# Kernel optimization log

Hardware: AMD Instinct MI355X
Metric: run time of the kernel (lower is better)

## Reference

```python
import jax, jax.numpy as jnp
import numpy as np

N, E, B, A = 50000, 1600000, 16, 4096
DIN, D, K = 32, 64, 50
EPS_BN = 1e-5


def setup_inputs() -> dict:
    key = jax.random.key(0)
    ks = iter(jax.random.split(key, 80))
    def rn(shape, s=0.05):
        return jax.random.normal(next(ks), shape, jnp.float32) * s
    inp = {
        "x": jax.random.normal(next(ks), (N, DIN), jnp.float32),
        "edge_index": jax.random.randint(next(ks), (2, E), 0, N),
        "action_edges": jax.random.randint(next(ks), (B, A, 2), 0, N),
        "army_counts": jax.random.normal(next(ks), (B, A), jnp.float32),
        "edge_mask": jnp.ones((B, A), jnp.bool_),
    }
    def bn(prefix, c):
        inp[prefix + "_g"] = 1.0 + rn((c,))
        inp[prefix + "_b"] = rn((c,))
        inp[prefix + "_m"] = rn((c,))
        inp[prefix + "_v"] = 1.0 + jax.random.uniform(next(ks), (c,), jnp.float32) * 0.1
    for i, cin in ((1, DIN), (2, D), (3, D)):
        inp[f"s{i}_wl"] = rn((cin, D), 0.1)
        inp[f"s{i}_bl"] = rn((D,))
        inp[f"s{i}_wr"] = rn((cin, D), 0.1)
        bn(f"s{i}_bn", D)
    inp["pl_w1"] = rn((D, 32), 0.1); inp["pl_b1"] = rn((32,)); bn("pl_bn", 32)
    inp["pl_w2"] = rn((32, 1), 0.1); inp["pl_b2"] = rn((1,))
    inp["es_w1"] = rn((2 * D, 64), 0.1); inp["es_b1"] = rn((64,)); bn("es_bn", 64)
    inp["es_w2"] = rn((64, 1), 0.1); inp["es_b2"] = rn((1,))
    inp["as_w1"] = rn((2 * D, 64), 0.1); inp["as_b1"] = rn((64,)); bn("as_bn", 64)
    inp["as_w2"] = rn((64, K), 0.1); inp["as_b2"] = rn((K,))
    return inp


def _bn(h, g, b, m, v):
    # BatchNorm1d in eval mode (running stats); dropout is identity in eval
    return (h - m) * jax.lax.rsqrt(v + EPS_BN) * g + b


def _sage_layer(h, src, dst, wl, bl, wr, g, b, m, v):
    # PyG SAGEConv(mean aggr, normalize=True): out = lin_l(mean_j x_j) + lin_r(x)
    msum = jax.ops.segment_sum(h[src], dst, num_segments=N)          # [N, din]
    cnt = jax.ops.segment_sum(jnp.ones((src.shape[0], 1), h.dtype), dst, num_segments=N)
    mean = msum / jnp.maximum(cnt, 1.0)
    out = mean @ wl + bl + h @ wr                                     # [N, D]
    nrm = jnp.linalg.norm(out, axis=-1, keepdims=True)
    out = out / jnp.maximum(nrm, 1e-12)                               # F.normalize
    return jax.nn.relu(_bn(out, g, b, m, v))


def reference(x, edge_index, action_edges, army_counts, edge_mask,
              s1_wl, s1_bl, s1_wr, s1_bn_g, s1_bn_b, s1_bn_m, s1_bn_v,
              s2_wl, s2_bl, s2_wr, s2_bn_g, s2_bn_b, s2_bn_m, s2_bn_v,
              s3_wl, s3_bl, s3_wr, s3_bn_g, s3_bn_b, s3_bn_m, s3_bn_v,
              pl_w1, pl_b1, pl_bn_g, pl_bn_b, pl_bn_m, pl_bn_v, pl_w2, pl_b2,
              es_w1, es_b1, es_bn_g, es_bn_b, es_bn_m, es_bn_v, es_w2, es_b2,
              as_w1, as_b1, as_bn_g, as_bn_b, as_bn_m, as_bn_v, as_w2, as_b2):
    src_g, dst_g = edge_index[0], edge_index[1]
    h = _sage_layer(x, src_g, dst_g, s1_wl, s1_bl, s1_wr, s1_bn_g, s1_bn_b, s1_bn_m, s1_bn_v)
    h = _sage_layer(h, src_g, dst_g, s2_wl, s2_bl, s2_wr, s2_bn_g, s2_bn_b, s2_bn_m, s2_bn_v)
    h = _sage_layer(h, src_g, dst_g, s3_wl, s3_bl, s3_wr, s3_bn_g, s3_bn_b, s3_bn_m, s3_bn_v)
    ne = jnp.clip(h, -5.0, 5.0)                                       # [N, D]

    # placement head
    p = jax.nn.relu(_bn(ne @ pl_w1 + pl_b1, pl_bn_g, pl_bn_b, pl_bn_m, pl_bn_v))
    placement_logits = jnp.clip((p @ pl_w2 + pl_b2).squeeze(-1), -15.0, 15.0)  # [N]

    # action-edge scoring
    src = jnp.clip(action_edges[..., 0], 0, N - 1)                    # [B, A]
    tgt = jnp.clip(action_edges[..., 1], 0, N - 1)
    edge_embed = jnp.concatenate([ne[src], ne[tgt]], axis=-1)         # [B, A, 2D]
    ee = jnp.clip(edge_embed, -3.0, 3.0).reshape(-1, 2 * D)           # [B*A, 2D]

    e = jax.nn.relu(_bn(ee @ es_w1 + es_b1, es_bn_g, es_bn_b, es_bn_m, es_bn_v))
    attack_logits = (e @ es_w2 + es_b2).squeeze(-1).reshape(B, A)
    a = jax.nn.relu(_bn(ee @ as_w1 + as_b1, as_bn_g, as_bn_b, as_bn_m, as_bn_v))
    army_logits = (a @ as_w2 + as_b2).reshape(B, A, K)

    attack_logits = jnp.clip(attack_logits, -15.0, 15.0)
    army_logits = jnp.clip(army_logits, -15.0, 15.0)
    attack_logits = jnp.where(edge_mask, attack_logits, -1e9)
    army_logits = jnp.where(edge_mask[..., None], army_logits, -1e9)
    return placement_logits, attack_logits, army_logits
```

## Files before the change

### kernel.cpp

```cpp
#include <hip/hip_runtime.h>

#define NN 50000
#define EE 1600000
#define NBA 65536
#define KH 50

static __device__ __forceinline__ float clipf(float x, float lo, float hi) {
    return fminf(fmaxf(x, lo), hi);
}


__global__ void k_degree(const int* __restrict__ dst, int* __restrict__ cnt, int E) {
    int i = blockIdx.x * blockDim.x + threadIdx.x;
    int stride = gridDim.x * blockDim.x;
    for (; i < E; i += stride) atomicAdd(&cnt[dst[i]], 1);
}

__global__ void k_scan1(const int* __restrict__ cnt, int* __restrict__ part,
                        int* __restrict__ bsum, int n) {
    __shared__ int sm[256];
    int t = threadIdx.x;
    int i = blockIdx.x * 256 + t;
    int v = (i < n) ? cnt[i] : 0;
    sm[t] = v; __syncthreads();
#pragma unroll
    for (int off = 1; off < 256; off <<= 1) {
        int u = (t >= off) ? sm[t - off] : 0;
        __syncthreads();
        sm[t] += u;
        __syncthreads();
    }
    if (i < n) part[i] = sm[t];
    if (t == 255) bsum[blockIdx.x] = sm[255];
}

__global__ void k_scan2(int* __restrict__ bsum, int nb) {
    __shared__ int sm[256];
    int t = threadIdx.x;
    int v = (t < nb) ? bsum[t] : 0;
    sm[t] = v; __syncthreads();
#pragma unroll
    for (int off = 1; off < 256; off <<= 1) {
        int u = (t >= off) ? sm[t - off] : 0;
        __syncthreads();
        sm[t] += u;
        __syncthreads();
    }
    if (t < nb) bsum[t] = sm[t];
}

__global__ void k_scan3(const int* __restrict__ cnt, const int* __restrict__ part,
                        const int* __restrict__ bsum, int* __restrict__ row_off,
                        int* __restrict__ cursor, int n) {
    int i = blockIdx.x * 256 + threadIdx.x;
    if (i >= n) return;
    int base = (blockIdx.x > 0) ? bsum[blockIdx.x - 1] : 0;
    int incl = part[i] + base;
    row_off[i + 1] = incl;
    cursor[i] = incl - cnt[i];
    if (i == 0) row_off[0] = 0;
}

__global__ void k_scatter(const int* __restrict__ src, const int* __restrict__ dst,
                          int* __restrict__ cursor, int* __restrict__ csr, int E) {
    int i = blockIdx.x * blockDim.x + threadIdx.x;
    int stride = gridDim.x * blockDim.x;
    for (; i < E; i += stride) {
        int d = dst[i];
        int p = atomicAdd(&cursor[d], 1);
        csr[p] = src[i];
    }
}


template <int DIN>
__global__ void bd_agg(const float* __restrict__ hin, float* __restrict__ meanb,
                       const int* __restrict__ row_off, const int* __restrict__ csr) {
    int node = blockIdx.x;
    int c = threadIdx.x;
    if (c >= DIN) return;
    int r0 = row_off[node], r1 = row_off[node + 1];
    double acc = 0.0;
    for (int j = r0; j < r1; ++j) acc += (double)hin[csr[j] * DIN + c];
    double cntv = (double)(r1 - r0);
    meanb[node * DIN + c] = (float)(acc / fmax(cntv, 1.0));
}


template <int DIN>
__global__ void bd_mat(const float* __restrict__ hin, const float* __restrict__ meanb,
                       float* __restrict__ hout,
                       const float* __restrict__ wl, const float* __restrict__ bl,
                       const float* __restrict__ wr,
                       const float* __restrict__ g, const float* __restrict__ b,
                       const float* __restrict__ m, const float* __restrict__ v,
                       int isFinal) {
    __shared__ double s_mean[DIN], s_h[DIN], s_sq[64], s_nrm;
    int node = blockIdx.x;
    int c = threadIdx.x;
    if (c < DIN) {
        s_mean[c] = (double)meanb[node * DIN + c];
        s_h[c] = (double)hin[node * DIN + c];
    }
    __syncthreads();
    double out = (double)bl[c];
    for (int k = 0; k < DIN; ++k)
        out += s_mean[k] * (double)wl[k * 64 + c] + s_h[k] * (double)wr[k * 64 + c];
    s_sq[c] = out * out;
    __syncthreads();
    if (c == 0) {
        double ss = 0.0;
        for (int i = 0; i < 64; ++i) ss += s_sq[i];
        s_nrm = fmax(sqrt(ss), 1e-12);
    }
    __syncthreads();
    double o = out / s_nrm;
    double y = ((o - (double)m[c]) * (1.0 / sqrt((double)v[c] + 1e-5))) * (double)g[c] + (double)b[c];
    y = fmax(y, 0.0);
    if (isFinal) y = fmin(y, 5.0);
    hout[node * 64 + c] = (float)y;
}


__global__ void bd_place(const float* __restrict__ ne,
                         const float* __restrict__ w1, const float* __restrict__ b1,
                         const float* __restrict__ g, const float* __restrict__ b,
                         const float* __restrict__ m, const float* __restrict__ v,
                         const float* __restrict__ w2, const float* __restrict__ b2,
                         float* __restrict__ out, int n) {
    int node = blockIdx.x * 256 + threadIdx.x;
    if (node >= n) return;
    double p = 0.0;
    for (int c = 0; c < 32; ++c) {
        double acc = (double)b1[c];
        for (int k = 0; k < 64; ++k) acc += (double)ne[node * 64 + k] * (double)w1[k * 32 + c];
        double y = ((acc - (double)m[c]) * (1.0 / sqrt((double)v[c] + 1e-5))) * (double)g[c] + (double)b[c];
        y = fmax(y, 0.0);
        p += y * (double)w2[c];
    }
    p += (double)b2[0];
    out[node] = (float)fmin(fmax(p, -15.0), 15.0);
}


__global__ __launch_bounds__(256) void k3_attack(const float* __restrict__ ne,
                                                 const int* __restrict__ ae,
                                                 const int* __restrict__ mask,
                                                 const float* __restrict__ w1,
                                                 const float* __restrict__ b1,
                                                 const float* __restrict__ g,
                                                 const float* __restrict__ b,
                                                 const float* __restrict__ m,
                                                 const float* __restrict__ v,
                                                 const float* __restrict__ w2,
                                                 const float* __restrict__ b2,
                                                 float* __restrict__ out, int nE) {
    __shared__ __align__(16) float s_w1[128 * 64];
    __shared__ __align__(16) float s_ee[4][4][128];
    for (int i = threadIdx.x; i < 128 * 64; i += 256) s_w1[i] = w1[i];
    __syncthreads();
    int wave = threadIdx.x >> 6, lane = threadIdx.x & 63;
    float b1_c = b1[lane];
    double scd = (double)g[lane] / sqrt((double)v[lane] + 1e-5);
    float scale = (float)scd;
    float shift = (float)((double)b[lane] - (double)m[lane] * scd);
    float w2_c = w2[lane], b2v = b2[0];
    int nwaves = (gridDim.x * blockDim.x) >> 6;
    for (int e0 = (blockIdx.x * 4 + wave) * 4; e0 < nE; e0 += nwaves * 4) {
#pragma unroll
        for (int q = 0; q < 4; ++q) {
            int e = min(e0 + q, nE - 1);
            int s = min(max(ae[e * 2 + 0], 0), NN - 1);
            int t = min(max(ae[e * 2 + 1], 0), NN - 1);
            s_ee[wave][q][lane] = clipf(ne[s * 64 + lane], -3.f, 3.f);
            s_ee[wave][q][64 + lane] = clipf(ne[t * 64 + lane], -3.f, 3.f);
        }
        float a[4] = {b1_c, b1_c, b1_c, b1_c};
#pragma unroll 8
        for (int k0 = 0; k0 < 128; k0 += 4) {
            float w_0 = s_w1[(k0 + 0) * 64 + lane];
            float w_1 = s_w1[(k0 + 1) * 64 + lane];
            float w_2 = s_w1[(k0 + 2) * 64 + lane];
            float w_3 = s_w1[(k0 + 3) * 64 + lane];
#pragma unroll
            for (int q = 0; q < 4; ++q) {
                float4 ev = *reinterpret_cast<const float4*>(&s_ee[wave][q][k0]);
                a[q] = fmaf(ev.x, w_0, a[q]);
                a[q] = fmaf(ev.y, w_1, a[q]);
                a[q] = fmaf(ev.z, w_2, a[q]);
                a[q] = fmaf(ev.w, w_3, a[q]);
            }
        }
#pragma unroll
        for (int q = 0; q < 4; ++q) {
            float y = fmaxf(fmaf(a[q], scale, shift), 0.f);
            float p = y * w2_c;
#pragma unroll
            for (int i = 32; i >= 1; i >>= 1) p += __shfl_xor(p, i);
            int e = e0 + q;
            if (lane == 0 && e < nE) {
                float logit = clipf(p + b2v, -15.f, 15.f);
                out[e] = mask[e] ? logit : -1e9f;
            }
        }
    }
}


__global__ __launch_bounds__(256) void k3_army(const float* __restrict__ ne,
                                               const int* __restrict__ ae,
                                               const int* __restrict__ mask,
                                               const float* __restrict__ w1,
                                               const float* __restrict__ b1,
                                               const float* __restrict__ g,
                                               const float* __restrict__ b,
                                               const float* __restrict__ m,
                                               const float* __restrict__ v,
                                               const float* __restrict__ w2,
                                               const float* __restrict__ b2,
                                               float* __restrict__ out, int nE) {
    __shared__ __align__(16) float s_w1[128 * 64];
    __shared__ __align__(16) float s_w2[64 * KH];
    __shared__ __align__(16) float s_ee[4][4][128];
    __shared__ __align__(16) double s_h[4][4][64];
    for (int i = threadIdx.x; i < 128 * 64; i += 256) s_w1[i] = w1[i];
    for (int i = threadIdx.x; i < 64 * KH; i += 256) s_w2[i] = w2[i];
    __syncthreads();
    int wave = threadIdx.x >> 6, lane = threadIdx.x & 63;
    double b1_c = (double)b1[lane];
    double m_c = (double)m[lane], g_c = (double)g[lane], b_c = (double)b[lane];
    double rsq = 1.0 / sqrt((double)v[lane] + 1e-5);
    double b2_k = (lane < KH) ? (double)b2[lane] : 0.0;
    int nwaves = (gridDim.x * blockDim.x) >> 6;
    for (int e0 = (blockIdx.x * 4 + wave) * 4; e0 < nE; e0 += nwaves * 4) {
#pragma unroll
        for (int q = 0; q < 4; ++q) {
            int e = min(e0 + q, nE - 1);
            int s = min(max(ae[e * 2 + 0], 0), NN - 1);
            int t = min(max(ae[e * 2 + 1], 0), NN - 1);
            s_ee[wave][q][lane] = clipf(ne[s * 64 + lane], -3.f, 3.f);
            s_ee[wave][q][64 + lane] = clipf(ne[t * 64 + lane], -3.f, 3.f);
        }
        double a[4] = {b1_c, b1_c, b1_c, b1_c};
#pragma unroll 4
        for (int k0 = 0; k0 < 128; k0 += 4) {
            double w_0 = (double)s_w1[(k0 + 0) * 64 + lane];
            double w_1 = (double)s_w1[(k0 + 1) * 64 + lane];
            double w_2 = (double)s_w1[(k0 + 2) * 64 + lane];
            double w_3 = (double)s_w1[(k0 + 3) * 64 + lane];
#pragma unroll
            for (int q = 0; q < 4; ++q) {
                float4 ev = *reinterpret_cast<const float4*>(&s_ee[wave][q][k0]);
                a[q] += (double)ev.x * w_0;
                a[q] += (double)ev.y * w_1;
                a[q] += (double)ev.z * w_2;
                a[q] += (double)ev.w * w_3;
            }
        }
#pragma unroll
        for (int q = 0; q < 4; ++q) {
            double hR = ((a[q] - m_c) * rsq) * g_c + b_c;
            s_h[wave][q][lane] = fmax(hR, 0.0);
        }
        double acc2[4] = {b2_k, b2_k, b2_k, b2_k};
        for (int j = 0; j < 64; ++j) {
            double w2j = (double)s_w2[j * KH + lane];
#pragma unroll
            for (int q = 0; q < 4; ++q) acc2[q] += s_h[wave][q][j] * w2j;
        }
#pragma unroll
        for (int q = 0; q < 4; ++q) {
            int e = e0 + q;
            if (lane < KH && e < nE) {
                float logit = (float)fmin(fmax(acc2[q], -15.0), 15.0);
                out[e * KH + lane] = mask[e] ? logit : -1e9f;
            }
        }
    }
}


extern "C" void kernel_launch(void* const* d_in, const int* in_sizes, int n_in,
                              void* d_out, int out_size, void* d_ws, size_t ws_size,
                              hipStream_t stream) {
    const float* x = (const float*)d_in[0];
    const int* ei = (const int*)d_in[1];
    const int* ae = (const int*)d_in[2];
    const int* mask = (const int*)d_in[4];
    const float *s1_wl = (const float*)d_in[5], *s1_bl = (const float*)d_in[6],
                *s1_wr = (const float*)d_in[7], *s1_g = (const float*)d_in[8],
                *s1_b = (const float*)d_in[9], *s1_m = (const float*)d_in[10],
                *s1_v = (const float*)d_in[11];
    const float *s2_wl = (const float*)d_in[12], *s2_bl = (const float*)d_in[13],
                *s2_wr = (const float*)d_in[14], *s2_g = (const float*)d_in[15],
                *s2_b = (const float*)d_in[16], *s2_m = (const float*)d_in[17],
                *s2_v = (const float*)d_in[18];
    const float *s3_wl = (const float*)d_in[19], *s3_bl = (const float*)d_in[20],
                *s3_wr = (const float*)d_in[21], *s3_g = (const float*)d_in[22],
                *s3_b = (const float*)d_in[23], *s3_m = (const float*)d_in[24],
                *s3_v = (const float*)d_in[25];
    const float *pl_w1 = (const float*)d_in[26], *pl_b1 = (const float*)d_in[27],
                *pl_g = (const float*)d_in[28], *pl_b = (const float*)d_in[29],
                *pl_m = (const float*)d_in[30], *pl_v = (const float*)d_in[31],
                *pl_w2 = (const float*)d_in[32], *pl_b2 = (const float*)d_in[33];
    const float *es_w1 = (const float*)d_in[34], *es_b1 = (const float*)d_in[35],
                *es_g = (const float*)d_in[36], *es_b = (const float*)d_in[37],
                *es_m = (const float*)d_in[38], *es_v = (const float*)d_in[39],
                *es_w2 = (const float*)d_in[40], *es_b2 = (const float*)d_in[41];
    const float *as_w1 = (const float*)d_in[42], *as_b1 = (const float*)d_in[43],
                *as_g = (const float*)d_in[44], *as_b = (const float*)d_in[45],
                *as_m = (const float*)d_in[46], *as_v = (const float*)d_in[47],
                *as_w2 = (const float*)d_in[48], *as_b2 = (const float*)d_in[49];

    char* w = (char*)d_ws;
    size_t off = 0;
    auto carve = [&](size_t bytes) {
        char* p = w + off;
        off = (off + bytes + 255) & ~(size_t)255;
        return p;
    };
    int* cnt = (int*)carve(NN * 4);
    int* part = (int*)carve(NN * 4);
    int* bsum = (int*)carve(256 * 4);
    int* row_off = (int*)carve((NN + 1) * 4);
    int* cursor = (int*)carve(NN * 4);
    int* csr = (int*)carve((size_t)EE * 4);
    float* meanb = (float*)carve((size_t)NN * 64 * 4);
    float* hA = (float*)carve((size_t)NN * 64 * 4);
    float* hB = (float*)carve((size_t)NN * 64 * 4);

    const int* src_g = ei;
    const int* dst_g = ei + EE;
    int nscan = (NN + 255) / 256;

    hipMemsetAsync(cnt, 0, NN * 4, stream);
    k_degree<<<1024, 256, 0, stream>>>(dst_g, cnt, EE);
    k_scan1<<<nscan, 256, 0, stream>>>(cnt, part, bsum, NN);
    k_scan2<<<1, 256, 0, stream>>>(bsum, nscan);
    k_scan3<<<nscan, 256, 0, stream>>>(cnt, part, bsum, row_off, cursor, NN);
    k_scatter<<<1024, 256, 0, stream>>>(src_g, dst_g, cursor, csr, EE);

    bd_agg<32><<<NN, 64, 0, stream>>>(x, meanb, row_off, csr);
    bd_mat<32><<<NN, 64, 0, stream>>>(x, meanb, hA, s1_wl, s1_bl, s1_wr,
                                      s1_g, s1_b, s1_m, s1_v, 0);
    bd_agg<64><<<NN, 64, 0, stream>>>(hA, meanb, row_off, csr);
    bd_mat<64><<<NN, 64, 0, stream>>>(hA, meanb, hB, s2_wl, s2_bl, s2_wr,
                                      s2_g, s2_b, s2_m, s2_v, 0);
    bd_agg<64><<<NN, 64, 0, stream>>>(hB, meanb, row_off, csr);
    bd_mat<64><<<NN, 64, 0, stream>>>(hB, meanb, hA, s3_wl, s3_bl, s3_wr,
                                      s3_g, s3_b, s3_m, s3_v, 1);
    const float* ne = hA;

    float* out_place = (float*)d_out;
    float* out_attack = out_place + NN;
    float* out_army = out_attack + NBA;

    bd_place<<<(NN + 255) / 256, 256, 0, stream>>>(ne, pl_w1, pl_b1, pl_g, pl_b,
                                                   pl_m, pl_v, pl_w2, pl_b2,
                                                   out_place, NN);
    k3_attack<<<1024, 256, 0, stream>>>(ne, ae, mask, es_w1, es_b1, es_g, es_b,
                                        es_m, es_v, es_w2, es_b2, out_attack, NBA);
    k3_army<<<1024, 256, 0, stream>>>(ne, ae, mask, as_w1, as_b1, as_g, as_b,
                                      as_m, as_v, as_w2, as_b2, out_army, NBA);
}
```

Measured before the change: 1.086 ms.

## Switch graph and head kernels to wave-per-node persistent grids with register weights

Replaces the one-block-per-node aggregation and SAGE matmul kernels with persistent wave-per-node kernels. The matmul weights are held in registers and the row norm is computed with wave shuffles instead of shared memory and block barriers. The placement head moves from a thread-per-node double-precision loop to a wave-per-node float kernel with weights staged in shared memory. The attack and army heads stop staging W1/W2 in shared memory and read them from global/L2 instead, with min-occupancy launch bounds. These changes aim to cut launch and barrier overhead and raise occupancy, at the cost of more register pressure and global weight traffic, and the placement head now runs in float instead of double.

```diff
diff --git a/kernel.cpp b/kernel.cpp
--- a/kernel.cpp
+++ b/kernel.cpp
@@ -74,142 +74,75 @@
 
 
 template <int DIN>
-__global__ void bd_agg(const float* __restrict__ hin, float* __restrict__ meanb,
-                       const int* __restrict__ row_off, const int* __restrict__ csr) {
-    int node = blockIdx.x;
-    int c = threadIdx.x;
-    if (c >= DIN) return;
-    int r0 = row_off[node], r1 = row_off[node + 1];
-    double acc = 0.0;
-    for (int j = r0; j < r1; ++j) acc += (double)hin[csr[j] * DIN + c];
-    double cntv = (double)(r1 - r0);
-    meanb[node * DIN + c] = (float)(acc / fmax(cntv, 1.0));
+__global__ __launch_bounds__(256) void k5_agg(const float* __restrict__ hin,
+                                              float* __restrict__ meanb,
+                                              const int* __restrict__ row_off,
+                                              const int* __restrict__ csr, int n) {
+    int wave = threadIdx.x >> 6, lane = threadIdx.x & 63;
+    int nw = (gridDim.x * blockDim.x) >> 6;
+    for (int node = blockIdx.x * 4 + wave; node < n; node += nw) {
+        int r0 = row_off[node], r1 = row_off[node + 1];
+        if (lane < DIN) {
+            double acc = 0.0;
+#pragma unroll 4
+            for (int j = r0; j < r1; ++j) {
+                int s = csr[j];
+                acc += (double)hin[s * DIN + lane];
+            }
+            meanb[node * DIN + lane] = (float)(acc / fmax((double)(r1 - r0), 1.0));
+        }
+    }
 }
 
 
 template <int DIN>
-__global__ void bd_mat(const float* __restrict__ hin, const float* __restrict__ meanb,
-                       float* __restrict__ hout,
-                       const float* __restrict__ wl, const float* __restrict__ bl,
-                       const float* __restrict__ wr,
-                       const float* __restrict__ g, const float* __restrict__ b,
-                       const float* __restrict__ m, const float* __restrict__ v,
-                       int isFinal) {
-    __shared__ double s_mean[DIN], s_h[DIN], s_sq[64], s_nrm;
-    int node = blockIdx.x;
-    int c = threadIdx.x;
-    if (c < DIN) {
-        s_mean[c] = (double)meanb[node * DIN + c];
-        s_h[c] = (double)hin[node * DIN + c];
-    }
-    __syncthreads();
-    double out = (double)bl[c];
-    for (int k = 0; k < DIN; ++k)
-        out += s_mean[k] * (double)wl[k * 64 + c] + s_h[k] * (double)wr[k * 64 + c];
-    s_sq[c] = out * out;
-    __syncthreads();
-    if (c == 0) {
-        double ss = 0.0;
-        for (int i = 0; i < 64; ++i) ss += s_sq[i];
-        s_nrm = fmax(sqrt(ss), 1e-12);
-    }
-    __syncthreads();
-    double o = out / s_nrm;
-    double y = ((o - (double)m[c]) * (1.0 / sqrt((double)v[c] + 1e-5))) * (double)g[c] + (double)b[c];
-    y = fmax(y, 0.0);
-    if (isFinal) y = fmin(y, 5.0);
-    hout[node * 64 + c] = (float)y;
-}
-
-
-__global__ void bd_place(const float* __restrict__ ne,
-                         const float* __restrict__ w1, const float* __restrict__ b1,
-                         const float* __restrict__ g, const float* __restrict__ b,
-                         const float* __restrict__ m, const float* __restrict__ v,
-                         const float* __restrict__ w2, const float* __restrict__ b2,
-                         float* __restrict__ out, int n) {
-    int node = blockIdx.x * 256 + threadIdx.x;
-    if (node >= n) return;
-    double p = 0.0;
-    for (int c = 0; c < 32; ++c) {
-        double acc = (double)b1[c];
-        for (int k = 0; k < 64; ++k) acc += (double)ne[node * 64 + k] * (double)w1[k * 32 + c];
-        double y = ((acc - (double)m[c]) * (1.0 / sqrt((double)v[c] + 1e-5))) * (double)g[c] + (double)b[c];
+__global__ __launch_bounds__(256) void k5_mat(const float* __restrict__ hin,
+                                              const float* __restrict__ meanb,
+                                              float* __restrict__ hout,
+                                              const float* __restrict__ wl,
+                                              const float* __restrict__ bl,
+                                              const float* __restrict__ wr,
+                                              const float* __restrict__ g,
+                                              const float* __restrict__ b,
+                                              const float* __restrict__ m,
+                                              const float* __restrict__ v,
+                                              int n, int isFinal) {
+    __shared__ __align__(16) float s_in[4][2][DIN];
+    int wave = threadIdx.x >> 6, lane = threadIdx.x & 63;
+    float wlc[DIN], wrc[DIN];
+#pragma unroll
+    for (int k = 0; k < DIN; ++k) {
+        wlc[k] = wl[k * 64 + lane];
+        wrc[k] = wr[k * 64 + lane];
+    }
+    double bl_d = (double)bl[lane];
+    double m_c = (double)m[lane], g_c = (double)g[lane], b_c = (double)b[lane];
+    double rsq = 1.0 / sqrt((double)v[lane] + 1e-5);
+    int nw = (gridDim.x * blockDim.x) >> 6;
+    for (int node = blockIdx.x * 4 + wave; node < n; node += nw) {
+        if (lane < DIN) {
+            s_in[wave][0][lane] = meanb[node * DIN + lane];
+            s_in[wave][1][lane] = hin[node * DIN + lane];
+        }
+        double out = bl_d;
+#pragma unroll 8
+        for (int k = 0; k < DIN; ++k)
+            out += (double)s_in[wave][0][k] * (double)wlc[k] +
+                   (double)s_in[wave][1][k] * (double)wrc[k];
+        double ss = out * out;
+#pragma unroll
+        for (int i = 32; i >= 1; i >>= 1) ss += __shfl_xor(ss, i);
+        double nrm = fmax(sqrt(ss), 1e-12);
+        double o = out / nrm;
+        double y = ((o - m_c) * rsq) * g_c + b_c;
         y = fmax(y, 0.0);
-        p += y * (double)w2[c];
-    }
-    p += (double)b2[0];
-    out[node] = (float)fmin(fmax(p, -15.0), 15.0);
-}
-
-
-__global__ __launch_bounds__(256) void k3_attack(const float* __restrict__ ne,
-                                                 const int* __restrict__ ae,
-                                                 const int* __restrict__ mask,
-                                                 const float* __restrict__ w1,
-                                                 const float* __restrict__ b1,
-                                                 const float* __restrict__ g,
-                                                 const float* __restrict__ b,
-                                                 const float* __restrict__ m,
-                                                 const float* __restrict__ v,
-                                                 const float* __restrict__ w2,
-                                                 const float* __restrict__ b2,
-                                                 float* __restrict__ out, int nE) {
-    __shared__ __align__(16) float s_w1[128 * 64];
-    __shared__ __align__(16) float s_ee[4][4][128];
-    for (int i = threadIdx.x; i < 128 * 64; i += 256) s_w1[i] = w1[i];
-    __syncthreads();
-    int wave = threadIdx.x >> 6, lane = threadIdx.x & 63;
-    float b1_c = b1[lane];
-    double scd = (double)g[lane] / sqrt((double)v[lane] + 1e-5);
-    float scale = (float)scd;
-    float shift = (float)((double)b[lane] - (double)m[lane] * scd);
-    float w2_c = w2[lane], b2v = b2[0];
-    int nwaves = (gridDim.x * blockDim.x) >> 6;
-    for (int e0 = (blockIdx.x * 4 + wave) * 4; e0 < nE; e0 += nwaves * 4) {
-#pragma unroll
-        for (int q = 0; q < 4; ++q) {
-            int e = min(e0 + q, nE - 1);
-            int s = min(max(ae[e * 2 + 0], 0), NN - 1);
-            int t = min(max(ae[e * 2 + 1], 0), NN - 1);
-            s_ee[wave][q][lane] = clipf(ne[s * 64 + lane], -3.f, 3.f);
-            s_ee[wave][q][64 + lane] = clipf(ne[t * 64 + lane], -3.f, 3.f);
-        }
-        float a[4] = {b1_c, b1_c, b1_c, b1_c};
-#pragma unroll 8
-        for (int k0 = 0; k0 < 128; k0 += 4) {
-            float w_0 = s_w1[(k0 + 0) * 64 + lane];
-            float w_1 = s_w1[(k0 + 1) * 64 + lane];
-            float w_2 = s_w1[(k0 + 2) * 64 + lane];
-            float w_3 = s_w1[(k0 + 3) * 64 + lane];
-#pragma unroll
-            for (int q = 0; q < 4; ++q) {
-                float4 ev = *reinterpret_cast<const float4*>(&s_ee[wave][q][k0]);
-                a[q] = fmaf(ev.x, w_0, a[q]);
-                a[q] = fmaf(ev.y, w_1, a[q]);
-                a[q] = fmaf(ev.z, w_2, a[q]);
-                a[q] = fmaf(ev.w, w_3, a[q]);
-            }
-        }
-#pragma unroll
-        for (int q = 0; q < 4; ++q) {
-            float y = fmaxf(fmaf(a[q], scale, shift), 0.f);
-            float p = y * w2_c;
-#pragma unroll
-            for (int i = 32; i >= 1; i >>= 1) p += __shfl_xor(p, i);
-            int e = e0 + q;
-            if (lane == 0 && e < nE) {
-                float logit = clipf(p + b2v, -15.f, 15.f);
-                out[e] = mask[e] ? logit : -1e9f;
-            }
-        }
-    }
-}
-
-
-__global__ __launch_bounds__(256) void k3_army(const float* __restrict__ ne,
-                                               const int* __restrict__ ae,
-                                               const int* __restrict__ mask,
+        if (isFinal) y = fmin(y, 5.0);
+        hout[node * 64 + lane] = (float)y;
+    }
+}
+
+
+__global__ __launch_bounds__(256) void k_place(const float* __restrict__ ne,
                                                const float* __restrict__ w1,
                                                const float* __restrict__ b1,
                                                const float* __restrict__ g,
@@ -218,14 +151,110 @@
                                                const float* __restrict__ v,
                                                const float* __restrict__ w2,
                                                const float* __restrict__ b2,
-                                               float* __restrict__ out, int nE) {
-    __shared__ __align__(16) float s_w1[128 * 64];
-    __shared__ __align__(16) float s_w2[64 * KH];
+                                               float* __restrict__ out, int n) {
+    __shared__ __align__(16) float s_w1[64 * 32];
+    __shared__ __align__(16) float s_row[4][64];
+    for (int i = threadIdx.x; i < 64 * 32; i += 256) s_w1[i] = w1[i];
+    __syncthreads();
+    int wave = threadIdx.x >> 6, lane = threadIdx.x & 63;
+    int c = lane & 31;
+    float b1_c = b1[c], w2_c = w2[c], b2v = b2[0];
+    float scale = g[c] * rsqrtf(v[c] + 1e-5f);
+    float shift = b[c] - m[c] * scale;
+    int nw = (gridDim.x * blockDim.x) >> 6;
+    for (int node = blockIdx.x * 4 + wave; node < n; node += nw) {
+        s_row[wave][lane] = ne[node * 64 + lane];
+        int k0 = (lane >> 5) * 32;
+        float acc = 0.f;
+#pragma unroll
+        for (int kk = 0; kk < 32; kk += 4) {
+            int k = k0 + kk;
+            float4 rv = *(const float4*)&s_row[wave][k];
+            acc += rv.x * s_w1[k * 32 + c] + rv.y * s_w1[(k + 1) * 32 + c] +
+                   rv.z * s_w1[(k + 2) * 32 + c] + rv.w * s_w1[(k + 3) * 32 + c];
+        }
+        acc += __shfl_xor(acc, 32);
+        float h = fmaxf((acc + b1_c) * scale + shift, 0.f);
+        float p = h * w2_c;
+#pragma unroll
+        for (int i = 16; i >= 1; i >>= 1) p += __shfl_xor(p, i);
+        if (lane == 0) out[node] = clipf(p + b2v, -15.f, 15.f);
+    }
+}
+
+
+__global__ __launch_bounds__(256, 4) void k6_attack(const float* __restrict__ ne,
+                                                    const int* __restrict__ ae,
+                                                    const int* __restrict__ mask,
+                                                    const float* __restrict__ w1,
+                                                    const float* __restrict__ b1,
+                                                    const float* __restrict__ g,
+                                                    const float* __restrict__ b,
+                                                    const float* __restrict__ m,
+                                                    const float* __restrict__ v,
+                                                    const float* __restrict__ w2,
+                                                    const float* __restrict__ b2,
+                                                    float* __restrict__ out, int nE) {
+    __shared__ __align__(16) float s_ee[4][4][128];
+    int wave = threadIdx.x >> 6, lane = threadIdx.x & 63;
+    float b1_c = b1[lane];
+    double scd = (double)g[lane] / sqrt((double)v[lane] + 1e-5);
+    float scale = (float)scd;
+    float shift = (float)((double)b[lane] - (double)m[lane] * scd);
+    float w2_c = w2[lane], b2v = b2[0];
+    int nwaves = (gridDim.x * blockDim.x) >> 6;
+    for (int e0 = (blockIdx.x * 4 + wave) * 4; e0 < nE; e0 += nwaves * 4) {
+#pragma unroll
+        for (int q = 0; q < 4; ++q) {
+            int e = min(e0 + q, nE - 1);
+            int s = min(max(ae[e * 2 + 0], 0), NN - 1);
+            int t = min(max(ae[e * 2 + 1], 0), NN - 1);
+            s_ee[wave][q][lane] = clipf(ne[s * 64 + lane], -3.f, 3.f);
+            s_ee[wave][q][64 + lane] = clipf(ne[t * 64 + lane], -3.f, 3.f);
+        }
+        float a[4] = {b1_c, b1_c, b1_c, b1_c};
+#pragma unroll 2
+        for (int k0 = 0; k0 < 128; k0 += 2) {
+            float w_0 = w1[(k0 + 0) * 64 + lane];
+            float w_1 = w1[(k0 + 1) * 64 + lane];
+#pragma unroll
+            for (int q = 0; q < 4; ++q) {
+                float e0v = s_ee[wave][q][k0 + 0];
+                float e1v = s_ee[wave][q][k0 + 1];
+                a[q] = fmaf(e0v, w_0, a[q]);
+                a[q] = fmaf(e1v, w_1, a[q]);
+            }
+        }
+#pragma unroll
+        for (int q = 0; q < 4; ++q) {
+            float y = fmaxf(fmaf(a[q], scale, shift), 0.f);
+            float p = y * w2_c;
+#pragma unroll
+            for (int i = 32; i >= 1; i >>= 1) p += __shfl_xor(p, i);
+            int e = e0 + q;
+            if (lane == 0 && e < nE) {
+                float logit = clipf(p + b2v, -15.f, 15.f);
+                out[e] = mask[e] ? logit : -1e9f;
+            }
+        }
+    }
+}
+
+
+__global__ __launch_bounds__(256, 4) void k6_army(const float* __restrict__ ne,
+                                                  const int* __restrict__ ae,
+                                                  const int* __restrict__ mask,
+                                                  const float* __restrict__ w1,
+                                                  const float* __restrict__ b1,
+                                                  const float* __restrict__ g,
+                                                  const float* __restrict__ b,
+                                                  const float* __restrict__ m,
+                                                  const float* __restrict__ v,
+                                                  const float* __restrict__ w2,
+                                                  const float* __restrict__ b2,
+                                                  float* __restrict__ out, int nE) {
     __shared__ __align__(16) float s_ee[4][4][128];
     __shared__ __align__(16) double s_h[4][4][64];
-    for (int i = threadIdx.x; i < 128 * 64; i += 256) s_w1[i] = w1[i];
-    for (int i = threadIdx.x; i < 64 * KH; i += 256) s_w2[i] = w2[i];
-    __syncthreads();
     int wave = threadIdx.x >> 6, lane = threadIdx.x & 63;
     double b1_c = (double)b1[lane];
     double m_c = (double)m[lane], g_c = (double)g[lane], b_c = (double)b[lane];
@@ -242,19 +271,16 @@
             s_ee[wave][q][64 + lane] = clipf(ne[t * 64 + lane], -3.f, 3.f);
         }
         double a[4] = {b1_c, b1_c, b1_c, b1_c};
-#pragma unroll 4
-        for (int k0 = 0; k0 < 128; k0 += 4) {
-            double w_0 = (double)s_w1[(k0 + 0) * 64 + lane];
-            double w_1 = (double)s_w1[(k0 + 1) * 64 + lane];
-            double w_2 = (double)s_w1[(k0 + 2) * 64 + lane];
-            double w_3 = (double)s_w1[(k0 + 3) * 64 + lane];
+#pragma unroll 2
+        for (int k0 = 0; k0 < 128; k0 += 2) {
+            double w_0 = (double)w1[(k0 + 0) * 64 + lane];
+            double w_1 = (double)w1[(k0 + 1) * 64 + lane];
 #pragma unroll
             for (int q = 0; q < 4; ++q) {
-                float4 ev = *reinterpret_cast<const float4*>(&s_ee[wave][q][k0]);
-                a[q] += (double)ev.x * w_0;
-                a[q] += (double)ev.y * w_1;
-                a[q] += (double)ev.z * w_2;
-                a[q] += (double)ev.w * w_3;
+                float e0v = s_ee[wave][q][k0 + 0];
+                float e1v = s_ee[wave][q][k0 + 1];
+                a[q] += (double)e0v * w_0;
+                a[q] += (double)e1v * w_1;
             }
         }
 #pragma unroll
@@ -264,7 +290,7 @@
         }
         double acc2[4] = {b2_k, b2_k, b2_k, b2_k};
         for (int j = 0; j < 64; ++j) {
-            double w2j = (double)s_w2[j * KH + lane];
+            double w2j = (lane < KH) ? (double)w2[j * KH + lane] : 0.0;
 #pragma unroll
             for (int q = 0; q < 4; ++q) acc2[q] += s_h[wave][q][j] * w2j;
         }
@@ -340,26 +366,25 @@
     k_scan3<<<nscan, 256, 0, stream>>>(cnt, part, bsum, row_off, cursor, NN);
     k_scatter<<<1024, 256, 0, stream>>>(src_g, dst_g, cursor, csr, EE);
 
-    bd_agg<32><<<NN, 64, 0, stream>>>(x, meanb, row_off, csr);
-    bd_mat<32><<<NN, 64, 0, stream>>>(x, meanb, hA, s1_wl, s1_bl, s1_wr,
-                                      s1_g, s1_b, s1_m, s1_v, 0);
-    bd_agg<64><<<NN, 64, 0, stream>>>(hA, meanb, row_off, csr);
-    bd_mat<64><<<NN, 64, 0, stream>>>(hA, meanb, hB, s2_wl, s2_bl, s2_wr,
-                                      s2_g, s2_b, s2_m, s2_v, 0);
-    bd_agg<64><<<NN, 64, 0, stream>>>(hB, meanb, row_off, csr);
-    bd_mat<64><<<NN, 64, 0, stream>>>(hB, meanb, hA, s3_wl, s3_bl, s3_wr,
-                                      s3_g, s3_b, s3_m, s3_v, 1);
+    k5_agg<32><<<2048, 256, 0, stream>>>(x, meanb, row_off, csr, NN);
+    k5_mat<32><<<2048, 256, 0, stream>>>(x, meanb, hA, s1_wl, s1_bl, s1_wr,
+                                         s1_g, s1_b, s1_m, s1_v, NN, 0);
+    k5_agg<64><<<2048, 256, 0, stream>>>(hA, meanb, row_off, csr, NN);
+    k5_mat<64><<<2048, 256, 0, stream>>>(hA, meanb, hB, s2_wl, s2_bl, s2_wr,
+                                         s2_g, s2_b, s2_m, s2_v, NN, 0);
+    k5_agg<64><<<2048, 256, 0, stream>>>(hB, meanb, row_off, csr, NN);
+    k5_mat<64><<<2048, 256, 0, stream>>>(hB, meanb, hA, s3_wl, s3_bl, s3_wr,
+                                         s3_g, s3_b, s3_m, s3_v, NN, 1);
     const float* ne = hA;
 
     float* out_place = (float*)d_out;
     float* out_attack = out_place + NN;
     float* out_army = out_attack + NBA;
 
-    bd_place<<<(NN + 255) / 256, 256, 0, stream>>>(ne, pl_w1, pl_b1, pl_g, pl_b,
-                                                   pl_m, pl_v, pl_w2, pl_b2,
-                                                   out_place, NN);
-    k3_attack<<<1024, 256, 0, stream>>>(ne, ae, mask, es_w1, es_b1, es_g, es_b,
+    k_place<<<2048, 256, 0, stream>>>(ne, pl_w1, pl_b1, pl_g, pl_b, pl_m, pl_v,
+                                      pl_w2, pl_b2, out_place, NN);
+    k6_attack<<<2048, 256, 0, stream>>>(ne, ae, mask, es_w1, es_b1, es_g, es_b,
                                         es_m, es_v, es_w2, es_b2, out_attack, NBA);
-    k3_army<<<1024, 256, 0, stream>>>(ne, ae, mask, as_w1, as_b1, as_g, as_b,
+    k6_army<<<2048, 256, 0, stream>>>(ne, ae, mask, as_w1, as_b1, as_g, as_b,
                                       as_m, as_v, as_w2, as_b2, out_army, NBA);
 }
```

After: 1.289 ms. +18.7%, slower.
